# Optimization experiments

Hardware: AMD Instinct MI355X
Metric: run time of the kernel (lower is better)

Reference implementation:

```python
import jax, jax.numpy as jnp
import numpy as np

N = 50000      # nodes
E = 1000000    # edges
B = 512        # graphs in batch
F = 32         # num_node_features
D = 64         # hidden_dim1
ED = 16        # edge_dim (8 edge_attr + 8 edge_feature)
STEPS = 3      # set2set processing steps


def setup_inputs() -> dict:
    key = jax.random.key(0)
    ks = jax.random.split(key, 24)
    rn = lambda k, shp, s=0.05: jax.random.normal(k, shp, dtype=jnp.float32) * s
    z = lambda *shp: jnp.zeros(shp, jnp.float32)
    inp = {}
    inp["x"] = jax.random.normal(ks[0], (N, F), dtype=jnp.float32)
    inp["edge_attr"] = jax.random.normal(ks[1], (E, 8), dtype=jnp.float32)
    inp["edge_feature"] = jax.random.normal(ks[2], (E, 8), dtype=jnp.float32)
    inp["edge_index"] = jax.random.randint(ks[3], (2, E), 0, N, dtype=jnp.int32)
    inp["batch"] = jnp.sort(jax.random.randint(ks[4], (N,), 0, B, dtype=jnp.int32))
    # conv0: GINEConv with nn = Linear(F,D)-ReLU-Linear(D,D); edge lin: ED -> F
    inp["conv0_ew"] = rn(ks[5], (ED, F)); inp["conv0_eb"] = z(F)
    inp["conv0_w1"] = rn(ks[6], (F, D));  inp["conv0_b1"] = z(D)
    inp["conv0_w2"] = rn(ks[7], (D, D));  inp["conv0_b2"] = z(D)
    # conv1: nn = Linear(D,D)-ReLU-Linear(D,D); edge lin: ED -> D
    inp["conv1_ew"] = rn(ks[8], (ED, D)); inp["conv1_eb"] = z(D)
    inp["conv1_w1"] = rn(ks[9], (D, D));  inp["conv1_b1"] = z(D)
    inp["conv1_w2"] = rn(ks[10], (D, D)); inp["conv1_b2"] = z(D)
    # Set2Set LSTM: input 2D -> hidden D (torch gate order i,f,g,o)
    inp["lstm_wih"] = rn(ks[11], (4 * D, 2 * D)); inp["lstm_bih"] = z(4 * D)
    inp["lstm_whh"] = rn(ks[12], (4 * D, D));     inp["lstm_bhh"] = z(4 * D)
    # dense head
    inp["dense_w"] = rn(ks[13], (2 * D, D)); inp["dense_b"] = z(D)
    inp["out_w"] = rn(ks[14], (D, 1));       inp["out_b"] = z(1)
    return inp


def _gine_conv(x, src, dst, eattr, ew, eb, w1, b1, w2, b2):
    # message = relu(x_j + lin(edge_attr)); sum-aggregate at target; eps=0
    msg = jax.nn.relu(x[src] + eattr @ ew + eb)          # [E, C]
    agg = jax.ops.segment_sum(msg, dst, num_segments=N)   # [N, C]
    h = x + agg                                            # (1+eps)*x + agg, eps=0
    return jax.nn.relu(h @ w1 + b1) @ w2 + b2


def _set2set(x, batch, wih, whh, bih, bhh):
    d = x.shape[1]
    q_star = jnp.zeros((B, 2 * d), x.dtype)
    h = jnp.zeros((B, d), x.dtype)
    c = jnp.zeros((B, d), x.dtype)
    for _ in range(STEPS):
        gates = q_star @ wih.T + bih + h @ whh.T + bhh     # [B, 4d]
        i, f, g, o = jnp.split(gates, 4, axis=1)
        c = jax.nn.sigmoid(f) * c + jax.nn.sigmoid(i) * jnp.tanh(g)
        h = jax.nn.sigmoid(o) * jnp.tanh(c)
        q = h                                              # [B, d]
        e = jnp.sum(x * q[batch], axis=-1)                 # [N]
        m = jax.ops.segment_max(e, batch, num_segments=B)
        ex = jnp.exp(e - m[batch])
        denom = jax.ops.segment_sum(ex, batch, num_segments=B)
        a = ex / denom[batch]                              # segmented softmax
        r = jax.ops.segment_sum(a[:, None] * x, batch, num_segments=B)  # [B, d]
        q_star = jnp.concatenate([q, r], axis=-1)
    return q_star


def reference(x, edge_attr, edge_feature, edge_index, batch,
              conv0_ew, conv0_eb, conv0_w1, conv0_b1, conv0_w2, conv0_b2,
              conv1_ew, conv1_eb, conv1_w1, conv1_b1, conv1_w2, conv1_b2,
              lstm_wih, lstm_whh, lstm_bih, lstm_bhh,
              dense_w, dense_b, out_w, out_b):
    ea = jnp.concatenate([edge_attr, edge_feature], axis=1)  # [E, ED]
    src, dst = edge_index[0], edge_index[1]
    h = jax.nn.relu(_gine_conv(x, src, dst, ea, conv0_ew, conv0_eb,
                               conv0_w1, conv0_b1, conv0_w2, conv0_b2))
    h = jax.nn.relu(_gine_conv(h, src, dst, ea, conv1_ew, conv1_eb,
                               conv1_w1, conv1_b1, conv1_w2, conv1_b2))
    pooled = _set2set(h, batch, lstm_wih, lstm_whh, lstm_bih, lstm_bhh)  # [B, 2D]
    z = jax.nn.relu(pooled @ dense_w + dense_b)
    return (z @ out_w + out_b)[:, 0]
```

## Files before the change

kernel.cpp:

```cpp
#include <hip/hip_runtime.h>
#include <math.h>

#define NN 50000
#define EE 1000000
#define BB 512

__device__ __forceinline__ float sigmoidf_(float x) { return 1.0f / (1.0f + __expf(-x)); }

__device__ __forceinline__ float uload(const float* p) {
    return __uint_as_float(__builtin_amdgcn_readfirstlane(__float_as_uint(*p)));
}
__device__ __forceinline__ int uloadi(const int* p) {
    return __builtin_amdgcn_readfirstlane(*p);
}

__global__ __launch_bounds__(256) void rank_kernel(const int* __restrict__ ei,
                                                   int* __restrict__ counts,
                                                   int* __restrict__ rnk)
{
    int e = blockIdx.x * 256 + threadIdx.x;
    if (e < EE) rnk[e] = atomicAdd(&counts[ei[EE + e]], 1);
}

__global__ __launch_bounds__(1024) void scan_kernel(const int* __restrict__ counts,
                                                    int* __restrict__ rowptr)
{
    __shared__ int s[1024];
    int t = threadIdx.x;
    const int CH = (NN + 1023) / 1024;
    int lo = t * CH, hi = lo + CH < NN ? lo + CH : NN;
    int sum = 0;
    for (int i = lo; i < hi; ++i) sum += counts[i];
    s[t] = sum;
    __syncthreads();
    for (int off = 1; off < 1024; off <<= 1) {
        int v = (t >= off) ? s[t - off] : 0;
        __syncthreads();
        s[t] += v;
        __syncthreads();
    }
    int base = (t > 0) ? s[t - 1] : 0;
    for (int i = lo; i < hi; ++i) { rowptr[i] = base; base += counts[i]; }
    if (t == 1023) rowptr[NN] = s[1023];
}

__global__ __launch_bounds__(256) void pack_kernel(
    const int* __restrict__ ei, const int* __restrict__ rnk,
    const int* __restrict__ rowptr,
    const float* __restrict__ eattr, const float* __restrict__ efeat,
    int* __restrict__ srcp, float* __restrict__ ea16)
{
    int e = blockIdx.x * 256 + threadIdx.x;
    if (e >= EE) return;
    int pos = rowptr[ei[EE + e]] + rnk[e];
    srcp[pos] = ei[e];
    const float4* pa = reinterpret_cast<const float4*>(eattr) + (size_t)e * 2;
    const float4* pf = reinterpret_cast<const float4*>(efeat) + (size_t)e * 2;
    float4* o = reinterpret_cast<float4*>(ea16 + (size_t)pos * 16);
    o[0] = pa[0]; o[1] = pa[1]; o[2] = pf[0]; o[3] = pf[1];
}

__global__ __launch_bounds__(256) void pack_ids_kernel(
    const int* __restrict__ ei, const int* __restrict__ rnk,
    const int* __restrict__ rowptr, int* __restrict__ perm)
{
    int e = blockIdx.x * 256 + threadIdx.x;
    if (e < EE) perm[rowptr[ei[EE + e]] + rnk[e]] = e;
}

__global__ __launch_bounds__(256) void batch_bounds_kernel(const int* __restrict__ batch,
                                                           int* __restrict__ brow)
{
    int i = blockIdx.x * 256 + threadIdx.x;
    if (i >= NN) return;
    int bi = batch[i];
    int prev = (i == 0) ? -1 : batch[i - 1];
    for (int v = prev + 1; v <= bi; ++v) brow[v] = i;
    if (i == NN - 1) for (int v = bi + 1; v <= BB; ++v) brow[v] = NN;
}

__global__ __launch_bounds__(256) void transpose_w_kernel(const float* __restrict__ wih,
                                                          const float* __restrict__ whh,
                                                          float* __restrict__ wihT,
                                                          float* __restrict__ whhT)
{
    int i = blockIdx.x * 256 + threadIdx.x;
    if (i < 128 * 256) {
        int k = i >> 8, g = i & 255;
        wihT[i] = wih[g * 128 + k];
    } else if (i < 192 * 256) {
        int j = i - 128 * 256;
        int k = j >> 8, g = j & 255;
        whhT[j] = whh[g * 64 + k];
    }
}

template <int CIN, bool PACKED>
__global__ __launch_bounds__(256) void gine_fused_kernel(
    const float* __restrict__ xin, const int* __restrict__ ei,
    const int* __restrict__ pidx,
    const int* __restrict__ rowptr,
    const float* __restrict__ eattr, const float* __restrict__ efeat,
    const float* __restrict__ ea16,
    const float* __restrict__ ew, const float* __restrict__ eb,
    const float* __restrict__ w1, const float* __restrict__ b1,
    const float* __restrict__ w2, const float* __restrict__ b2,
    float* __restrict__ hout)
{
    __shared__ float w1_lds[CIN * 64];
    for (int i = threadIdx.x; i < CIN * 64; i += 256) w1_lds[i] = w1[i];
    __syncthreads();

    int wave = threadIdx.x >> 6, lane = threadIdx.x & 63;
    int node = blockIdx.x * 4 + wave;
    if (node >= NN) return;

    int ch = lane & (CIN - 1);

    float wreg[16];
#pragma unroll
    for (int k = 0; k < 16; ++k) wreg[k] = ew[k * CIN + ch];
    float ebv = eb[ch];

    int start = rowptr[node], end = rowptr[node + 1];
    float agg = 0.0f;

    auto fetch16 = [&](int slot, float* a) -> int {
        if constexpr (PACKED) {
            int src = uloadi(pidx + slot);
            const float* p = ea16 + (size_t)slot * 16;
#pragma unroll
            for (int k = 0; k < 16; ++k) a[k] = uload(p + k);
            return src;
        } else {
            int e = uloadi(pidx + slot);
            int src = uloadi(ei + e);
            const float* pa = eattr + (size_t)e * 8;
            const float* pf = efeat + (size_t)e * 8;
#pragma unroll
            for (int k = 0; k < 8; ++k) { a[k] = uload(pa + k); a[8 + k] = uload(pf + k); }
            return src;
        }
    };

    if constexpr (CIN == 64) {
        int j = start;
        for (; j + 3 < end; j += 4) {
            int jb = __builtin_amdgcn_readfirstlane(j);
            float a0[16], a1[16], a2[16], a3[16];
            int s0 = fetch16(jb, a0);
            int s1 = fetch16(jb + 1, a1);
            int s2 = fetch16(jb + 2, a2);
            int s3 = fetch16(jb + 3, a3);
            float m0 = xin[(size_t)s0 * 64 + lane] + ebv;
            float m1 = xin[(size_t)s1 * 64 + lane] + ebv;
            float m2 = xin[(size_t)s2 * 64 + lane] + ebv;
            float m3 = xin[(size_t)s3 * 64 + lane] + ebv;
#pragma unroll
            for (int k = 0; k < 16; ++k) {
                m0 += a0[k] * wreg[k];
                m1 += a1[k] * wreg[k];
                m2 += a2[k] * wreg[k];
                m3 += a3[k] * wreg[k];
            }
            agg += fmaxf(m0, 0.0f) + fmaxf(m1, 0.0f)
                 + fmaxf(m2, 0.0f) + fmaxf(m3, 0.0f);
        }
        for (; j < end; ++j) {
            int jb = __builtin_amdgcn_readfirstlane(j);
            float a0[16];
            int s0 = fetch16(jb, a0);
            float m0 = xin[(size_t)s0 * 64 + lane] + ebv;
#pragma unroll
            for (int k = 0; k < 16; ++k) m0 += a0[k] * wreg[k];
            agg += fmaxf(m0, 0.0f);
        }
    } else {
        int half = lane >> 5;
        int j = start;
        for (; j + 1 < end; j += 2) {
            int jb = __builtin_amdgcn_readfirstlane(j);
            float a0[16], a1[16];
            int s0 = fetch16(jb, a0);
            int s1 = fetch16(jb + 1, a1);
            float xv = xin[(size_t)(half ? s1 : s0) * 32 + ch];
            float m0 = 0.0f, m1 = 0.0f;
#pragma unroll
            for (int k = 0; k < 16; ++k) {
                m0 += a0[k] * wreg[k];
                m1 += a1[k] * wreg[k];
            }
            float m = half ? m1 : m0;
            agg += fmaxf(xv + m + ebv, 0.0f);
        }
        if (j < end) {
            int jb = __builtin_amdgcn_readfirstlane(j);
            float a0[16];
            int s0 = fetch16(jb, a0);
            float xv = xin[(size_t)s0 * 32 + ch];
            float m0 = 0.0f;
#pragma unroll
            for (int k = 0; k < 16; ++k) m0 += a0[k] * wreg[k];
            agg += (half == 0) ? fmaxf(xv + m0 + ebv, 0.0f) : 0.0f;
        }
        agg += __shfl_xor(agg, 32);
    }

    float h_in = 0.0f;
    if (lane < CIN) h_in = xin[(size_t)node * CIN + lane] + agg;

    float hid = b1[lane];
#pragma unroll
    for (int i = 0; i < CIN; ++i)
        hid += __shfl(h_in, i) * w1_lds[i * 64 + lane];
    hid = fmaxf(hid, 0.0f);

    float o = b2[lane];
#pragma unroll
    for (int i = 0; i < 64; ++i)
        o += __shfl(hid, i) * w2[i * 64 + lane];

    hout[(size_t)node * 64 + lane] = fmaxf(o, 0.0f);
}

__global__ __launch_bounds__(1024) void set2set_head_v3(
    const float* __restrict__ h2, const int* __restrict__ brow,
    const float* __restrict__ wihT, const float* __restrict__ whhT,
    const float* __restrict__ bih, const float* __restrict__ bhh,
    const float* __restrict__ dw, const float* __restrict__ db,
    const float* __restrict__ ow, const float* __restrict__ ob,
    float* __restrict__ outp)
{
    int b = blockIdx.x, tid = threadIdx.x;
    int wv = tid >> 6, lane = tid & 63;
    __shared__ float qstar[128], hh[64], cc[64];
    __shared__ float gpart[4][256];
    __shared__ float redw[16][64];
    __shared__ float redm[16], reds[16];

    int start = brow[b], end = brow[b + 1];

    if (tid < 128) qstar[tid] = 0.0f;
    if (tid < 64) { hh[tid] = 0.0f; cc[tid] = 0.0f; }
    __syncthreads();

    for (int step = 0; step < 3; ++step) {
        {
            int p = tid >> 8, g = tid & 255;
            float acc = 0.0f;
            const float* wT = wihT + (size_t)(32 * p) * 256 + g;
#pragma unroll 8
            for (int k = 0; k < 32; ++k) acc += qstar[32 * p + k] * wT[(size_t)k * 256];
            const float* hT = whhT + (size_t)(16 * p) * 256 + g;
#pragma unroll 8
            for (int k = 0; k < 16; ++k) acc += hh[16 * p + k] * hT[(size_t)k * 256];
            gpart[p][g] = acc;
        }
        __syncthreads();
        if (tid < 64) {
            float gi = bih[tid]       + bhh[tid]       + gpart[0][tid]       + gpart[1][tid]       + gpart[2][tid]       + gpart[3][tid];
            float gf = bih[64 + tid]  + bhh[64 + tid]  + gpart[0][64 + tid]  + gpart[1][64 + tid]  + gpart[2][64 + tid]  + gpart[3][64 + tid];
            float gg = bih[128 + tid] + bhh[128 + tid] + gpart[0][128 + tid] + gpart[1][128 + tid] + gpart[2][128 + tid] + gpart[3][128 + tid];
            float go = bih[192 + tid] + bhh[192 + tid] + gpart[0][192 + tid] + gpart[1][192 + tid] + gpart[2][192 + tid] + gpart[3][192 + tid];
            float c = sigmoidf_(gf) * cc[tid] + sigmoidf_(gi) * tanhf(gg);
            cc[tid] = c;
            hh[tid] = sigmoidf_(go) * tanhf(c);
        }
        __syncthreads();

        float qv = hh[lane];
        float mw = -INFINITY, sw = 0.0f, rw = 0.0f;
        for (int n = start + wv; n < end; n += 16) {
            float v = h2[(size_t)n * 64 + lane];
            float p = v * qv;
#pragma unroll
            for (int off = 32; off; off >>= 1) p += __shfl_xor(p, off);
            float nm = fmaxf(mw, p);
            float sc = __expf(mw - nm);
            float pe = __expf(p - nm);
            sw = sw * sc + pe;
            rw = rw * sc + pe * v;
            mw = nm;
        }
        redm[wv] = mw; reds[wv] = sw; redw[wv][lane] = rw;
        __syncthreads();
        if (tid < 64) {
            float M = -INFINITY;
#pragma unroll
            for (int w = 0; w < 16; ++w) M = fmaxf(M, redm[w]);
            float S = 0.0f, R = 0.0f;
#pragma unroll
            for (int w = 0; w < 16; ++w) {
                float mm = redm[w];
                if (mm > -INFINITY) {
                    float sc = __expf(mm - M);
                    S += reds[w] * sc;
                    R += redw[w][tid] * sc;
                }
            }
            qstar[tid] = hh[tid];
            qstar[64 + tid] = (S > 0.0f) ? R / S : 0.0f;
        }
        __syncthreads();
    }

    if (tid < 64) {
        float z = db[tid];
#pragma unroll 4
        for (int k = 0; k < 128; ++k) z += qstar[k] * dw[k * 64 + tid];
        redw[0][tid] = fmaxf(z, 0.0f);
    }
    __syncthreads();
    if (tid < 64) {
        float t = redw[0][tid] * ow[tid];
#pragma unroll
        for (int off = 32; off; off >>= 1) t += __shfl_xor(t, off);
        if (tid == 0) outp[b] = t + ob[0];
    }
}

extern "C" void kernel_launch(void* const* d_in, const int* in_sizes, int n_in,
                              void* d_out, int out_size, void* d_ws, size_t ws_size,
                              hipStream_t stream)
{
    const float* x     = (const float*)d_in[0];
    const float* eattr = (const float*)d_in[1];
    const float* efeat = (const float*)d_in[2];
    const int*   ei    = (const int*)d_in[3];
    const int*   batch = (const int*)d_in[4];
    const float* c0_ew = (const float*)d_in[5];  const float* c0_eb = (const float*)d_in[6];
    const float* c0_w1 = (const float*)d_in[7];  const float* c0_b1 = (const float*)d_in[8];
    const float* c0_w2 = (const float*)d_in[9];  const float* c0_b2 = (const float*)d_in[10];
    const float* c1_ew = (const float*)d_in[11]; const float* c1_eb = (const float*)d_in[12];
    const float* c1_w1 = (const float*)d_in[13]; const float* c1_b1 = (const float*)d_in[14];
    const float* c1_w2 = (const float*)d_in[15]; const float* c1_b2 = (const float*)d_in[16];
    const float* wih   = (const float*)d_in[17]; const float* bih   = (const float*)d_in[18];
    const float* whh   = (const float*)d_in[19]; const float* bhh   = (const float*)d_in[20];
    const float* dw    = (const float*)d_in[21]; const float* dbias = (const float*)d_in[22];
    const float* ow    = (const float*)d_in[23]; const float* ob    = (const float*)d_in[24];

    float* out = (float*)d_out;
    int* iws = (int*)d_ws;

    int* counts = iws;
    int* rowptr = counts + NN;
    int* brow   = rowptr + NN + 1;
    size_t off0 = ((size_t)2 * NN + 1 + (BB + 1) + 15) & ~(size_t)15;
    float* wihT = (float*)(iws + off0);
    float* whhT = wihT + 128 * 256;
    int*   srcp = (int*)(whhT + 64 * 256);
    size_t offE = (off0 + 128 * 256 + 64 * 256 + EE + 15) & ~(size_t)15;
    float* ea16 = (float*)(iws + offE);
    float* h1   = ea16 + (size_t)EE * 16;
    float* h2   = h1 + (size_t)NN * 64;
    int*   rnk  = (int*)h1;
    const size_t needP = (offE + (size_t)EE * 16 + (size_t)NN * 128) * sizeof(int);

    hipMemsetAsync(counts, 0, (size_t)NN * sizeof(int), stream);
    batch_bounds_kernel<<<(NN + 255) / 256, 256, 0, stream>>>(batch, brow);
    transpose_w_kernel<<<192, 256, 0, stream>>>(wih, whh, wihT, whhT);

    if (ws_size >= needP) {
        rank_kernel<<<(EE + 255) / 256, 256, 0, stream>>>(ei, counts, rnk);
        scan_kernel<<<1, 1024, 0, stream>>>(counts, rowptr);
        pack_kernel<<<(EE + 255) / 256, 256, 0, stream>>>(
            ei, rnk, rowptr, eattr, efeat, srcp, ea16);
        gine_fused_kernel<32, true><<<(NN + 3) / 4, 256, 0, stream>>>(
            x, ei, srcp, rowptr, eattr, efeat, ea16,
            c0_ew, c0_eb, c0_w1, c0_b1, c0_w2, c0_b2, h1);
        gine_fused_kernel<64, true><<<(NN + 3) / 4, 256, 0, stream>>>(
            h1, ei, srcp, rowptr, eattr, efeat, ea16,
            c1_ew, c1_eb, c1_w1, c1_b1, c1_w2, c1_b2, h2);
    } else {
        int* perm = srcp;
        float* h1f = (float*)(iws + offE);
        float* h2f = h1f + (size_t)NN * 64;
        int* rnkf  = (int*)(h2f + (size_t)NN * 64);
        rank_kernel<<<(EE + 255) / 256, 256, 0, stream>>>(ei, counts, rnkf);
        scan_kernel<<<1, 1024, 0, stream>>>(counts, rowptr);
        pack_ids_kernel<<<(EE + 255) / 256, 256, 0, stream>>>(ei, rnkf, rowptr, perm);
        gine_fused_kernel<32, false><<<(NN + 3) / 4, 256, 0, stream>>>(
            x, ei, perm, rowptr, eattr, efeat, nullptr,
            c0_ew, c0_eb, c0_w1, c0_b1, c0_w2, c0_b2, h1f);
        gine_fused_kernel<64, false><<<(NN + 3) / 4, 256, 0, stream>>>(
            h1f, ei, perm, rowptr, eattr, efeat, nullptr,
            c1_ew, c1_eb, c1_w1, c1_b1, c1_w2, c1_b2, h2f);
        h2 = h2f;
    }

    set2set_head_v3<<<BB, 1024, 0, stream>>>(h2, brow, wihT, whhT, bih, bhh,
                                             dw, dbias, ow, ob, out);
}
```

Baseline: 408.4 us.

## Prefetch next neighbor features in GINE loop and merge setup kernels

The packed GINE aggregation loop now loads the source-node feature rows for the next group of edges while the current group's edge attributes are being processed. This software-pipelines the dependent gather latency. The memset, batch-bounds and weight-transpose launches are folded into one setup kernel to cut launch overhead. The cost is extra registers for the prefetched values, which may lower occupancy. The unpacked fallback path is simplified to handle one edge per iteration.

New measurement: 408.5 us. About the same (+0.0%).

```diff
diff --git a/kernel.cpp b/kernel.cpp
--- a/kernel.cpp
+++ b/kernel.cpp
@@ -12,6 +12,24 @@
 }
 __device__ __forceinline__ int uloadi(const int* p) {
     return __builtin_amdgcn_readfirstlane(*p);
+}
+
+__global__ __launch_bounds__(256) void setup_kernel(
+    const int* __restrict__ batch, int* __restrict__ brow,
+    const float* __restrict__ wih, const float* __restrict__ whh,
+    float* __restrict__ wihT, float* __restrict__ whhT,
+    int* __restrict__ counts)
+{
+    int i = blockIdx.x * 256 + threadIdx.x;
+    if (i < NN) {
+        counts[i] = 0;
+        int bi = batch[i];
+        int prev = (i == 0) ? -1 : batch[i - 1];
+        for (int v = prev + 1; v <= bi; ++v) brow[v] = i;
+        if (i == NN - 1) for (int v = bi + 1; v <= BB; ++v) brow[v] = NN;
+    }
+    if (i < 128 * 256) wihT[i] = wih[(i & 255) * 128 + (i >> 8)];
+    if (i < 64 * 256)  whhT[i] = whh[(i & 255) * 64 + (i >> 8)];
 }
 
 __global__ __launch_bounds__(256) void rank_kernel(const int* __restrict__ ei,
@@ -66,33 +84,6 @@
 {
     int e = blockIdx.x * 256 + threadIdx.x;
     if (e < EE) perm[rowptr[ei[EE + e]] + rnk[e]] = e;
-}
-
-__global__ __launch_bounds__(256) void batch_bounds_kernel(const int* __restrict__ batch,
-                                                           int* __restrict__ brow)
-{
-    int i = blockIdx.x * 256 + threadIdx.x;
-    if (i >= NN) return;
-    int bi = batch[i];
-    int prev = (i == 0) ? -1 : batch[i - 1];
-    for (int v = prev + 1; v <= bi; ++v) brow[v] = i;
-    if (i == NN - 1) for (int v = bi + 1; v <= BB; ++v) brow[v] = NN;
-}
-
-__global__ __launch_bounds__(256) void transpose_w_kernel(const float* __restrict__ wih,
-                                                          const float* __restrict__ whh,
-                                                          float* __restrict__ wihT,
-                                                          float* __restrict__ whhT)
-{
-    int i = blockIdx.x * 256 + threadIdx.x;
-    if (i < 128 * 256) {
-        int k = i >> 8, g = i & 255;
-        wihT[i] = wih[g * 128 + k];
-    } else if (i < 192 * 256) {
-        int j = i - 128 * 256;
-        int k = j >> 8, g = j & 255;
-        whhT[j] = whh[g * 64 + k];
-    }
 }
 
 template <int CIN, bool PACKED>
@@ -125,85 +116,128 @@
     int start = rowptr[node], end = rowptr[node + 1];
     float agg = 0.0f;
 
-    auto fetch16 = [&](int slot, float* a) -> int {
-        if constexpr (PACKED) {
-            int src = uloadi(pidx + slot);
-            const float* p = ea16 + (size_t)slot * 16;
-#pragma unroll
-            for (int k = 0; k < 16; ++k) a[k] = uload(p + k);
-            return src;
+    if constexpr (PACKED) {
+        if constexpr (CIN == 64) {
+            int nfull = (end - start) & ~3;
+            int jend4 = start + nfull;
+            int j = start;
+            float xc0, xc1, xc2, xc3;
+            if (j < jend4) {
+                int jb = __builtin_amdgcn_readfirstlane(j);
+                int s0 = uloadi(pidx + jb),     s1 = uloadi(pidx + jb + 1);
+                int s2 = uloadi(pidx + jb + 2), s3 = uloadi(pidx + jb + 3);
+                xc0 = xin[(size_t)s0 * 64 + lane];
+                xc1 = xin[(size_t)s1 * 64 + lane];
+                xc2 = xin[(size_t)s2 * 64 + lane];
+                xc3 = xin[(size_t)s3 * 64 + lane];
+            }
+            for (; j < jend4; j += 4) {
+                int jb = __builtin_amdgcn_readfirstlane(j);
+                bool more = (jb + 4) < jend4;
+                float xn0, xn1, xn2, xn3;
+                if (more) {
+                    int s0 = uloadi(pidx + jb + 4), s1 = uloadi(pidx + jb + 5);
+                    int s2 = uloadi(pidx + jb + 6), s3 = uloadi(pidx + jb + 7);
+                    xn0 = xin[(size_t)s0 * 64 + lane];
+                    xn1 = xin[(size_t)s1 * 64 + lane];
+                    xn2 = xin[(size_t)s2 * 64 + lane];
+                    xn3 = xin[(size_t)s3 * 64 + lane];
+                }
+                float a0[16], a1[16], a2[16], a3[16];
+                const float* p = ea16 + (size_t)jb * 16;
+#pragma unroll
+                for (int k = 0; k < 16; ++k) {
+                    a0[k] = uload(p + k);
+                    a1[k] = uload(p + 16 + k);
+                    a2[k] = uload(p + 32 + k);
+                    a3[k] = uload(p + 48 + k);
+                }
+                float m0 = xc0 + ebv, m1 = xc1 + ebv, m2 = xc2 + ebv, m3 = xc3 + ebv;
+#pragma unroll
+                for (int k = 0; k < 16; ++k) {
+                    m0 += a0[k] * wreg[k];
+                    m1 += a1[k] * wreg[k];
+                    m2 += a2[k] * wreg[k];
+                    m3 += a3[k] * wreg[k];
+                }
+                agg += fmaxf(m0, 0.0f) + fmaxf(m1, 0.0f)
+                     + fmaxf(m2, 0.0f) + fmaxf(m3, 0.0f);
+                if (more) { xc0 = xn0; xc1 = xn1; xc2 = xn2; xc3 = xn3; }
+            }
+            for (; j < end; ++j) {
+                int jb = __builtin_amdgcn_readfirstlane(j);
+                int s0 = uloadi(pidx + jb);
+                float m0 = xin[(size_t)s0 * 64 + lane] + ebv;
+                const float* p = ea16 + (size_t)jb * 16;
+#pragma unroll
+                for (int k = 0; k < 16; ++k) m0 += uload(p + k) * wreg[k];
+                agg += fmaxf(m0, 0.0f);
+            }
         } else {
-            int e = uloadi(pidx + slot);
-            int src = uloadi(ei + e);
+            int half = lane >> 5;
+            int nfull = (end - start) & ~1;
+            int jend2 = start + nfull;
+            int j = start;
+            float xc;
+            if (j < jend2) {
+                int jb = __builtin_amdgcn_readfirstlane(j);
+                int s0 = uloadi(pidx + jb), s1 = uloadi(pidx + jb + 1);
+                xc = xin[(size_t)(half ? s1 : s0) * 32 + ch];
+            }
+            for (; j < jend2; j += 2) {
+                int jb = __builtin_amdgcn_readfirstlane(j);
+                bool more = (jb + 2) < jend2;
+                float xn;
+                if (more) {
+                    int s0 = uloadi(pidx + jb + 2), s1 = uloadi(pidx + jb + 3);
+                    xn = xin[(size_t)(half ? s1 : s0) * 32 + ch];
+                }
+                float a0[16], a1[16];
+                const float* p = ea16 + (size_t)jb * 16;
+#pragma unroll
+                for (int k = 0; k < 16; ++k) {
+                    a0[k] = uload(p + k);
+                    a1[k] = uload(p + 16 + k);
+                }
+                float m0 = 0.0f, m1 = 0.0f;
+#pragma unroll
+                for (int k = 0; k < 16; ++k) {
+                    m0 += a0[k] * wreg[k];
+                    m1 += a1[k] * wreg[k];
+                }
+                agg += fmaxf(xc + (half ? m1 : m0) + ebv, 0.0f);
+                if (more) xc = xn;
+            }
+            if (j < end) {
+                int jb = __builtin_amdgcn_readfirstlane(j);
+                int s0 = uloadi(pidx + jb);
+                float xv = xin[(size_t)s0 * 32 + ch];
+                const float* p = ea16 + (size_t)jb * 16;
+                float m0 = 0.0f;
+#pragma unroll
+                for (int k = 0; k < 16; ++k) m0 += uload(p + k) * wreg[k];
+                agg += (half == 0) ? fmaxf(xv + m0 + ebv, 0.0f) : 0.0f;
+            }
+            agg += __shfl_xor(agg, 32);
+        }
+    } else {
+        for (int j = start; j < end; ++j) {
+            int jb = __builtin_amdgcn_readfirstlane(j);
+            int e = uloadi(pidx + jb);
+            int s0 = uloadi(ei + e);
+            float xv = xin[(size_t)s0 * CIN + ch];
             const float* pa = eattr + (size_t)e * 8;
             const float* pf = efeat + (size_t)e * 8;
-#pragma unroll
-            for (int k = 0; k < 8; ++k) { a[k] = uload(pa + k); a[8 + k] = uload(pf + k); }
-            return src;
-        }
-    };
-
-    if constexpr (CIN == 64) {
-        int j = start;
-        for (; j + 3 < end; j += 4) {
-            int jb = __builtin_amdgcn_readfirstlane(j);
-            float a0[16], a1[16], a2[16], a3[16];
-            int s0 = fetch16(jb, a0);
-            int s1 = fetch16(jb + 1, a1);
-            int s2 = fetch16(jb + 2, a2);
-            int s3 = fetch16(jb + 3, a3);
-            float m0 = xin[(size_t)s0 * 64 + lane] + ebv;
-            float m1 = xin[(size_t)s1 * 64 + lane] + ebv;
-            float m2 = xin[(size_t)s2 * 64 + lane] + ebv;
-            float m3 = xin[(size_t)s3 * 64 + lane] + ebv;
-#pragma unroll
-            for (int k = 0; k < 16; ++k) {
-                m0 += a0[k] * wreg[k];
-                m1 += a1[k] * wreg[k];
-                m2 += a2[k] * wreg[k];
-                m3 += a3[k] * wreg[k];
-            }
-            agg += fmaxf(m0, 0.0f) + fmaxf(m1, 0.0f)
-                 + fmaxf(m2, 0.0f) + fmaxf(m3, 0.0f);
-        }
-        for (; j < end; ++j) {
-            int jb = __builtin_amdgcn_readfirstlane(j);
-            float a0[16];
-            int s0 = fetch16(jb, a0);
-            float m0 = xin[(size_t)s0 * 64 + lane] + ebv;
-#pragma unroll
-            for (int k = 0; k < 16; ++k) m0 += a0[k] * wreg[k];
-            agg += fmaxf(m0, 0.0f);
-        }
-    } else {
-        int half = lane >> 5;
-        int j = start;
-        for (; j + 1 < end; j += 2) {
-            int jb = __builtin_amdgcn_readfirstlane(j);
-            float a0[16], a1[16];
-            int s0 = fetch16(jb, a0);
-            int s1 = fetch16(jb + 1, a1);
-            float xv = xin[(size_t)(half ? s1 : s0) * 32 + ch];
-            float m0 = 0.0f, m1 = 0.0f;
-#pragma unroll
-            for (int k = 0; k < 16; ++k) {
-                m0 += a0[k] * wreg[k];
-                m1 += a1[k] * wreg[k];
-            }
-            float m = half ? m1 : m0;
-            agg += fmaxf(xv + m + ebv, 0.0f);
-        }
-        if (j < end) {
-            int jb = __builtin_amdgcn_readfirstlane(j);
-            float a0[16];
-            int s0 = fetch16(jb, a0);
-            float xv = xin[(size_t)s0 * 32 + ch];
-            float m0 = 0.0f;
-#pragma unroll
-            for (int k = 0; k < 16; ++k) m0 += a0[k] * wreg[k];
-            agg += (half == 0) ? fmaxf(xv + m0 + ebv, 0.0f) : 0.0f;
-        }
-        agg += __shfl_xor(agg, 32);
+            float m0 = xv + ebv;
+#pragma unroll
+            for (int k = 0; k < 8; ++k) {
+                m0 += uload(pa + k) * wreg[k];
+                m0 += uload(pf + k) * wreg[8 + k];
+            }
+            if constexpr (CIN == 64) agg += fmaxf(m0, 0.0f);
+            else                      agg += (lane < 32) ? fmaxf(m0, 0.0f) : 0.0f;
+        }
+        if constexpr (CIN == 32) agg += __shfl_xor(agg, 32);
     }
 
     float h_in = 0.0f;
@@ -356,9 +390,8 @@
     int*   rnk  = (int*)h1;
     const size_t needP = (offE + (size_t)EE * 16 + (size_t)NN * 128) * sizeof(int);
 
-    hipMemsetAsync(counts, 0, (size_t)NN * sizeof(int), stream);
-    batch_bounds_kernel<<<(NN + 255) / 256, 256, 0, stream>>>(batch, brow);
-    transpose_w_kernel<<<192, 256, 0, stream>>>(wih, whh, wihT, whhT);
+    setup_kernel<<<(NN + 255) / 256, 256, 0, stream>>>(batch, brow, wih, whh,
+                                                       wihT, whhT, counts);
 
     if (ws_size >= needP) {
         rank_kernel<<<(EE + 255) / 256, 256, 0, stream>>>(ei, counts, rnk);
```

## Store node features and packed edge attributes in fp16, use dot2 accumulation

Applied to the files above, without the earlier changes.

Converts x, the packed edge attributes and the intermediate hidden features h1/h2 to fp16 storage. Edge linear projections use packed half dot2 instructions with fp32 accumulation. The memset, batch-bounds and weight-transpose launches are merged into one setup kernel, and the unpacked fallback path is removed. This halves the gather and edge-stream bytes in the memory-bound GINE kernels at the cost of reduced precision in intermediate activations.

Result: faster. 386.8 us (-5.3%).

```diff
diff --git a/kernel.cpp b/kernel.cpp
--- a/kernel.cpp
+++ b/kernel.cpp
@@ -5,13 +5,53 @@
 #define EE 1000000
 #define BB 512
 
+typedef _Float16 hf;
+typedef __attribute__((ext_vector_type(2))) _Float16 hf2;
+
 __device__ __forceinline__ float sigmoidf_(float x) { return 1.0f / (1.0f + __expf(-x)); }
 
-__device__ __forceinline__ float uload(const float* p) {
-    return __uint_as_float(__builtin_amdgcn_readfirstlane(__float_as_uint(*p)));
-}
 __device__ __forceinline__ int uloadi(const int* p) {
     return __builtin_amdgcn_readfirstlane(*p);
+}
+__device__ __forceinline__ unsigned uloadu(const unsigned* p) {
+    return (unsigned)__builtin_amdgcn_readfirstlane((int)*p);
+}
+
+__device__ __forceinline__ unsigned pack2(float a, float b) {
+    hf2 h; h.x = (_Float16)a; h.y = (_Float16)b;
+    return __builtin_bit_cast(unsigned, h);
+}
+
+__device__ __forceinline__ float dot2acc(unsigned au, hf2 w, float acc) {
+    hf2 a = __builtin_bit_cast(hf2, au);
+#if __has_builtin(__builtin_amdgcn_fdot2)
+    return __builtin_amdgcn_fdot2(a, w, acc, false);
+#else
+    return acc + (float)a.x * (float)w.x + (float)a.y * (float)w.y;
+#endif
+}
+
+__global__ __launch_bounds__(256) void setup_kernel(
+    const int* __restrict__ batch, int* __restrict__ brow,
+    const float* __restrict__ wih, const float* __restrict__ whh,
+    float* __restrict__ wihT, float* __restrict__ whhT,
+    int* __restrict__ counts, const float* __restrict__ x, unsigned* __restrict__ xh)
+{
+    int i = blockIdx.x * 256 + threadIdx.x;
+    if (i < NN) {
+        counts[i] = 0;
+        int bi = batch[i];
+        int prev = (i == 0) ? -1 : batch[i - 1];
+        for (int v = prev + 1; v <= bi; ++v) brow[v] = i;
+        if (i == NN - 1) for (int v = bi + 1; v <= BB; ++v) brow[v] = NN;
+    }
+    if (i < 128 * 256) wihT[i] = wih[(i & 255) * 128 + (i >> 8)];
+    if (i < 64 * 256)  whhT[i] = whh[(i & 255) * 64 + (i >> 8)];
+    if (i < NN * 8) {
+        float4 v = reinterpret_cast<const float4*>(x)[i];
+        uint2 o; o.x = pack2(v.x, v.y); o.y = pack2(v.z, v.w);
+        reinterpret_cast<uint2*>(xh)[i] = o;
+    }
 }
 
 __global__ __launch_bounds__(256) void rank_kernel(const int* __restrict__ ei,
@@ -48,7 +88,7 @@
     const int* __restrict__ ei, const int* __restrict__ rnk,
     const int* __restrict__ rowptr,
     const float* __restrict__ eattr, const float* __restrict__ efeat,
-    int* __restrict__ srcp, float* __restrict__ ea16)
+    int* __restrict__ srcp, unsigned* __restrict__ eah)
 {
     int e = blockIdx.x * 256 + threadIdx.x;
     if (e >= EE) return;
@@ -56,56 +96,24 @@
     srcp[pos] = ei[e];
     const float4* pa = reinterpret_cast<const float4*>(eattr) + (size_t)e * 2;
     const float4* pf = reinterpret_cast<const float4*>(efeat) + (size_t)e * 2;
-    float4* o = reinterpret_cast<float4*>(ea16 + (size_t)pos * 16);
-    o[0] = pa[0]; o[1] = pa[1]; o[2] = pf[0]; o[3] = pf[1];
-}
-
-__global__ __launch_bounds__(256) void pack_ids_kernel(
-    const int* __restrict__ ei, const int* __restrict__ rnk,
-    const int* __restrict__ rowptr, int* __restrict__ perm)
-{
-    int e = blockIdx.x * 256 + threadIdx.x;
-    if (e < EE) perm[rowptr[ei[EE + e]] + rnk[e]] = e;
-}
-
-__global__ __launch_bounds__(256) void batch_bounds_kernel(const int* __restrict__ batch,
-                                                           int* __restrict__ brow)
-{
-    int i = blockIdx.x * 256 + threadIdx.x;
-    if (i >= NN) return;
-    int bi = batch[i];
-    int prev = (i == 0) ? -1 : batch[i - 1];
-    for (int v = prev + 1; v <= bi; ++v) brow[v] = i;
-    if (i == NN - 1) for (int v = bi + 1; v <= BB; ++v) brow[v] = NN;
-}
-
-__global__ __launch_bounds__(256) void transpose_w_kernel(const float* __restrict__ wih,
-                                                          const float* __restrict__ whh,
-                                                          float* __restrict__ wihT,
-                                                          float* __restrict__ whhT)
-{
-    int i = blockIdx.x * 256 + threadIdx.x;
-    if (i < 128 * 256) {
-        int k = i >> 8, g = i & 255;
-        wihT[i] = wih[g * 128 + k];
-    } else if (i < 192 * 256) {
-        int j = i - 128 * 256;
-        int k = j >> 8, g = j & 255;
-        whhT[j] = whh[g * 64 + k];
-    }
-}
-
-template <int CIN, bool PACKED>
+    float4 v0 = pa[0], v1 = pa[1], v2 = pf[0], v3 = pf[1];
+    uint4 o0, o1;
+    o0.x = pack2(v0.x, v0.y); o0.y = pack2(v0.z, v0.w);
+    o0.z = pack2(v1.x, v1.y); o0.w = pack2(v1.z, v1.w);
+    o1.x = pack2(v2.x, v2.y); o1.y = pack2(v2.z, v2.w);
+    o1.z = pack2(v3.x, v3.y); o1.w = pack2(v3.z, v3.w);
+    uint4* o = reinterpret_cast<uint4*>(eah + (size_t)pos * 8);
+    o[0] = o0; o[1] = o1;
+}
+
+template <int CIN>
 __global__ __launch_bounds__(256) void gine_fused_kernel(
-    const float* __restrict__ xin, const int* __restrict__ ei,
-    const int* __restrict__ pidx,
-    const int* __restrict__ rowptr,
-    const float* __restrict__ eattr, const float* __restrict__ efeat,
-    const float* __restrict__ ea16,
+    const hf* __restrict__ xin, const int* __restrict__ pidx,
+    const int* __restrict__ rowptr, const unsigned* __restrict__ eah,
     const float* __restrict__ ew, const float* __restrict__ eb,
     const float* __restrict__ w1, const float* __restrict__ b1,
     const float* __restrict__ w2, const float* __restrict__ b2,
-    float* __restrict__ hout)
+    hf* __restrict__ hout)
 {
     __shared__ float w1_lds[CIN * 64];
     for (int i = threadIdx.x; i < CIN * 64; i += 256) w1_lds[i] = w1[i];
@@ -117,62 +125,53 @@
 
     int ch = lane & (CIN - 1);
 
-    float wreg[16];
-#pragma unroll
-    for (int k = 0; k < 16; ++k) wreg[k] = ew[k * CIN + ch];
+    hf2 wh[8];
+#pragma unroll
+    for (int k = 0; k < 8; ++k) {
+        wh[k].x = (_Float16)ew[(2 * k) * CIN + ch];
+        wh[k].y = (_Float16)ew[(2 * k + 1) * CIN + ch];
+    }
     float ebv = eb[ch];
 
     int start = rowptr[node], end = rowptr[node + 1];
     float agg = 0.0f;
-
-    auto fetch16 = [&](int slot, float* a) -> int {
-        if constexpr (PACKED) {
-            int src = uloadi(pidx + slot);
-            const float* p = ea16 + (size_t)slot * 16;
-#pragma unroll
-            for (int k = 0; k < 16; ++k) a[k] = uload(p + k);
-            return src;
-        } else {
-            int e = uloadi(pidx + slot);
-            int src = uloadi(ei + e);
-            const float* pa = eattr + (size_t)e * 8;
-            const float* pf = efeat + (size_t)e * 8;
-#pragma unroll
-            for (int k = 0; k < 8; ++k) { a[k] = uload(pa + k); a[8 + k] = uload(pf + k); }
-            return src;
-        }
-    };
 
     if constexpr (CIN == 64) {
         int j = start;
         for (; j + 3 < end; j += 4) {
             int jb = __builtin_amdgcn_readfirstlane(j);
-            float a0[16], a1[16], a2[16], a3[16];
-            int s0 = fetch16(jb, a0);
-            int s1 = fetch16(jb + 1, a1);
-            int s2 = fetch16(jb + 2, a2);
-            int s3 = fetch16(jb + 3, a3);
-            float m0 = xin[(size_t)s0 * 64 + lane] + ebv;
-            float m1 = xin[(size_t)s1 * 64 + lane] + ebv;
-            float m2 = xin[(size_t)s2 * 64 + lane] + ebv;
-            float m3 = xin[(size_t)s3 * 64 + lane] + ebv;
-#pragma unroll
-            for (int k = 0; k < 16; ++k) {
-                m0 += a0[k] * wreg[k];
-                m1 += a1[k] * wreg[k];
-                m2 += a2[k] * wreg[k];
-                m3 += a3[k] * wreg[k];
+            int s0 = uloadi(pidx + jb),     s1 = uloadi(pidx + jb + 1);
+            int s2 = uloadi(pidx + jb + 2), s3 = uloadi(pidx + jb + 3);
+            float m0 = (float)xin[(size_t)s0 * 64 + lane] + ebv;
+            float m1 = (float)xin[(size_t)s1 * 64 + lane] + ebv;
+            float m2 = (float)xin[(size_t)s2 * 64 + lane] + ebv;
+            float m3 = (float)xin[(size_t)s3 * 64 + lane] + ebv;
+            const unsigned* p = eah + (size_t)jb * 8;
+            unsigned a0[8], a1[8], a2[8], a3[8];
+#pragma unroll
+            for (int k = 0; k < 8; ++k) {
+                a0[k] = uloadu(p + k);
+                a1[k] = uloadu(p + 8 + k);
+                a2[k] = uloadu(p + 16 + k);
+                a3[k] = uloadu(p + 24 + k);
+            }
+#pragma unroll
+            for (int k = 0; k < 8; ++k) {
+                m0 = dot2acc(a0[k], wh[k], m0);
+                m1 = dot2acc(a1[k], wh[k], m1);
+                m2 = dot2acc(a2[k], wh[k], m2);
+                m3 = dot2acc(a3[k], wh[k], m3);
             }
             agg += fmaxf(m0, 0.0f) + fmaxf(m1, 0.0f)
                  + fmaxf(m2, 0.0f) + fmaxf(m3, 0.0f);
         }
         for (; j < end; ++j) {
             int jb = __builtin_amdgcn_readfirstlane(j);
-            float a0[16];
-            int s0 = fetch16(jb, a0);
-            float m0 = xin[(size_t)s0 * 64 + lane] + ebv;
-#pragma unroll
-            for (int k = 0; k < 16; ++k) m0 += a0[k] * wreg[k];
+            int s0 = uloadi(pidx + jb);
+            float m0 = (float)xin[(size_t)s0 * 64 + lane] + ebv;
+            const unsigned* p = eah + (size_t)jb * 8;
+#pragma unroll
+            for (int k = 0; k < 8; ++k) m0 = dot2acc(uloadu(p + k), wh[k], m0);
             agg += fmaxf(m0, 0.0f);
         }
     } else {
@@ -180,34 +179,36 @@
         int j = start;
         for (; j + 1 < end; j += 2) {
             int jb = __builtin_amdgcn_readfirstlane(j);
-            float a0[16], a1[16];
-            int s0 = fetch16(jb, a0);
-            int s1 = fetch16(jb + 1, a1);
-            float xv = xin[(size_t)(half ? s1 : s0) * 32 + ch];
+            int s0 = uloadi(pidx + jb);
+            int s1 = uloadi(pidx + jb + 1);
+            float xv = (float)xin[(size_t)(half ? s1 : s0) * 32 + ch];
+            const unsigned* p = eah + (size_t)jb * 8;
+            unsigned a0[8], a1[8];
+#pragma unroll
+            for (int k = 0; k < 8; ++k) { a0[k] = uloadu(p + k); a1[k] = uloadu(p + 8 + k); }
             float m0 = 0.0f, m1 = 0.0f;
 #pragma unroll
-            for (int k = 0; k < 16; ++k) {
-                m0 += a0[k] * wreg[k];
-                m1 += a1[k] * wreg[k];
+            for (int k = 0; k < 8; ++k) {
+                m0 = dot2acc(a0[k], wh[k], m0);
+                m1 = dot2acc(a1[k], wh[k], m1);
             }
-            float m = half ? m1 : m0;
-            agg += fmaxf(xv + m + ebv, 0.0f);
+            agg += fmaxf(xv + (half ? m1 : m0) + ebv, 0.0f);
         }
         if (j < end) {
             int jb = __builtin_amdgcn_readfirstlane(j);
-            float a0[16];
-            int s0 = fetch16(jb, a0);
-            float xv = xin[(size_t)s0 * 32 + ch];
+            int s0 = uloadi(pidx + jb);
+            float xv = (float)xin[(size_t)s0 * 32 + ch];
+            const unsigned* p = eah + (size_t)jb * 8;
             float m0 = 0.0f;
 #pragma unroll
-            for (int k = 0; k < 16; ++k) m0 += a0[k] * wreg[k];
+            for (int k = 0; k < 8; ++k) m0 = dot2acc(uloadu(p + k), wh[k], m0);
             agg += (half == 0) ? fmaxf(xv + m0 + ebv, 0.0f) : 0.0f;
         }
         agg += __shfl_xor(agg, 32);
     }
 
     float h_in = 0.0f;
-    if (lane < CIN) h_in = xin[(size_t)node * CIN + lane] + agg;
+    if (lane < CIN) h_in = (float)xin[(size_t)node * CIN + lane] + agg;
 
     float hid = b1[lane];
 #pragma unroll
@@ -220,11 +221,11 @@
     for (int i = 0; i < 64; ++i)
         o += __shfl(hid, i) * w2[i * 64 + lane];
 
-    hout[(size_t)node * 64 + lane] = fmaxf(o, 0.0f);
+    hout[(size_t)node * 64 + lane] = (hf)fmaxf(o, 0.0f);
 }
 
 __global__ __launch_bounds__(1024) void set2set_head_v3(
-    const float* __restrict__ h2, const int* __restrict__ brow,
+    const hf* __restrict__ h2, const int* __restrict__ brow,
     const float* __restrict__ wihT, const float* __restrict__ whhT,
     const float* __restrict__ bih, const float* __restrict__ bhh,
     const float* __restrict__ dw, const float* __restrict__ db,
@@ -271,7 +272,7 @@
         float qv = hh[lane];
         float mw = -INFINITY, sw = 0.0f, rw = 0.0f;
         for (int n = start + wv; n < end; n += 16) {
-            float v = h2[(size_t)n * 64 + lane];
+            float v = (float)h2[(size_t)n * 64 + lane];
             float p = v * qv;
 #pragma unroll
             for (int off = 32; off; off >>= 1) p += __shfl_xor(p, off);
@@ -349,45 +350,26 @@
     float* wihT = (float*)(iws + off0);
     float* whhT = wihT + 128 * 256;
     int*   srcp = (int*)(whhT + 64 * 256);
-    size_t offE = (off0 + 128 * 256 + 64 * 256 + EE + 15) & ~(size_t)15;
-    float* ea16 = (float*)(iws + offE);
-    float* h1   = ea16 + (size_t)EE * 16;
-    float* h2   = h1 + (size_t)NN * 64;
-    int*   rnk  = (int*)h1;
-    const size_t needP = (offE + (size_t)EE * 16 + (size_t)NN * 128) * sizeof(int);
-
-    hipMemsetAsync(counts, 0, (size_t)NN * sizeof(int), stream);
-    batch_bounds_kernel<<<(NN + 255) / 256, 256, 0, stream>>>(batch, brow);
-    transpose_w_kernel<<<192, 256, 0, stream>>>(wih, whh, wihT, whhT);
-
-    if (ws_size >= needP) {
-        rank_kernel<<<(EE + 255) / 256, 256, 0, stream>>>(ei, counts, rnk);
-        scan_kernel<<<1, 1024, 0, stream>>>(counts, rowptr);
-        pack_kernel<<<(EE + 255) / 256, 256, 0, stream>>>(
-            ei, rnk, rowptr, eattr, efeat, srcp, ea16);
-        gine_fused_kernel<32, true><<<(NN + 3) / 4, 256, 0, stream>>>(
-            x, ei, srcp, rowptr, eattr, efeat, ea16,
-            c0_ew, c0_eb, c0_w1, c0_b1, c0_w2, c0_b2, h1);
-        gine_fused_kernel<64, true><<<(NN + 3) / 4, 256, 0, stream>>>(
-            h1, ei, srcp, rowptr, eattr, efeat, ea16,
-            c1_ew, c1_eb, c1_w1, c1_b1, c1_w2, c1_b2, h2);
-    } else {
-        int* perm = srcp;
-        float* h1f = (float*)(iws + offE);
-        float* h2f = h1f + (size_t)NN * 64;
-        int* rnkf  = (int*)(h2f + (size_t)NN * 64);
-        rank_kernel<<<(EE + 255) / 256, 256, 0, stream>>>(ei, counts, rnkf);
-        scan_kernel<<<1, 1024, 0, stream>>>(counts, rowptr);
-        pack_ids_kernel<<<(EE + 255) / 256, 256, 0, stream>>>(ei, rnkf, rowptr, perm);
-        gine_fused_kernel<32, false><<<(NN + 3) / 4, 256, 0, stream>>>(
-            x, ei, perm, rowptr, eattr, efeat, nullptr,
-            c0_ew, c0_eb, c0_w1, c0_b1, c0_w2, c0_b2, h1f);
-        gine_fused_kernel<64, false><<<(NN + 3) / 4, 256, 0, stream>>>(
-            h1f, ei, perm, rowptr, eattr, efeat, nullptr,
-            c1_ew, c1_eb, c1_w1, c1_b1, c1_w2, c1_b2, h2f);
-        h2 = h2f;
-    }
-
-    set2set_head_v3<<<BB, 1024, 0, stream>>>(h2, brow, wihT, whhT, bih, bhh,
+    unsigned* xh = (unsigned*)(srcp + EE);
+    size_t offE = (off0 + 128 * 256 + 64 * 256 + EE + (size_t)NN * 16 + 15) & ~(size_t)15;
+    unsigned* eah = (unsigned*)(iws + offE);
+    hf* h1h = (hf*)(eah + (size_t)EE * 8);
+    hf* h2h = h1h + (size_t)NN * 64;
+    int* rnk = (int*)h1h;
+
+    int setup_grid = (NN * 8 + 255) / 256;
+    setup_kernel<<<setup_grid, 256, 0, stream>>>(batch, brow, wih, whh,
+                                                 wihT, whhT, counts, x, xh);
+    rank_kernel<<<(EE + 255) / 256, 256, 0, stream>>>(ei, counts, rnk);
+    scan_kernel<<<1, 1024, 0, stream>>>(counts, rowptr);
+    pack_kernel<<<(EE + 255) / 256, 256, 0, stream>>>(
+        ei, rnk, rowptr, eattr, efeat, srcp, eah);
+    gine_fused_kernel<32><<<(NN + 3) / 4, 256, 0, stream>>>(
+        (const hf*)xh, srcp, rowptr, eah,
+        c0_ew, c0_eb, c0_w1, c0_b1, c0_w2, c0_b2, h1h);
+    gine_fused_kernel<64><<<(NN + 3) / 4, 256, 0, stream>>>(
+        h1h, srcp, rowptr, eah,
+        c1_ew, c1_eb, c1_w1, c1_b1, c1_w2, c1_b2, h2h);
+    set2set_head_v3<<<BB, 1024, 0, stream>>>(h2h, brow, wihT, whhT, bih, bhh,
                                              dw, dbias, ow, ob, out);
 }
```
